# Kernel tuning notes

Measured on AMD Instinct MI355X. Metric: run time of the kernel, lower is better.

The kernel has to match this reference:

```python
import jax, jax.numpy as jnp
import numpy as np

ALPHA = 0.2  # LeakyReLU negative slope


def _gat_layer(h, dst, adj, w, a_in, a_out, b):
    # h: [N, F_in], dst: [N, K] int (edge (i,k): i -> dst[i,k]), adj: [N, K]
    hid = h @ w                      # [N, D]
    s_in = hid @ a_in                # [N]  (attention applied to source-node half)
    s_out = hid @ a_out              # [N]  (attention applied to dest-node half)
    # edge scores, grouped per source node (matches view(-1, num_neighs) softmax)
    e = jax.nn.leaky_relu(s_in[:, None] + s_out[dst], ALPHA)   # [N, K]
    # torch code detaches attention (Variable(..., requires_grad=False))
    att = jax.lax.stop_gradient(jax.nn.softmax(e, axis=1))     # [N, K]
    w_edge = adj * att                                          # [N, K]
    # SpMM: out[i] = sum_k w_edge[i,k] * hid[dst[i,k]]
    out = jnp.einsum('nk,nkd->nd', w_edge, hid[dst]) + b        # [N, D]
    return out


def setup_inputs() -> dict:
    key = jax.random.key(0)
    ks = jax.random.split(key, 12)
    N, K, F, H, O = 100000, 16, 128, 128, 128
    stdv1 = 1.0 / np.sqrt(H)
    stdv2 = 1.0 / np.sqrt(O)
    u = lambda k, shp, s: jax.random.uniform(k, shp, jnp.float32, -s, s)
    return {
        'x': jax.random.normal(ks[0], (N, F), jnp.float32),
        'dst_idx': jax.random.randint(ks[1], (N, K), 0, N),
        'adj_vals': jax.random.uniform(ks[2], (N, K), jnp.float32),
        'w1': u(ks[3], (F, H), stdv1),
        'a_in1': jax.random.normal(ks[4], (H,), jnp.float32) * (1.414 / np.sqrt(H)),
        'a_out1': jax.random.normal(ks[5], (H,), jnp.float32) * (1.414 / np.sqrt(H)),
        'b1': u(ks[6], (H,), stdv1),
        'w2': u(ks[7], (H, O), stdv2),
        'a_in2': jax.random.normal(ks[8], (O,), jnp.float32) * (1.414 / np.sqrt(O)),
        'a_out2': jax.random.normal(ks[9], (O,), jnp.float32) * (1.414 / np.sqrt(O)),
        'b2': u(ks[10], (O,), stdv2),
    }


def reference(x, dst_idx, adj_vals, w1, a_in1, a_out1, b1, w2, a_in2, a_out2, b2):
    h = jax.nn.relu(_gat_layer(x, dst_idx, adj_vals, w1, a_in1, a_out1, b1))
    h = jax.nn.relu(_gat_layer(h, dst_idx, adj_vals, w2, a_in2, a_out2, b2))
    return h
```

## Files before the change

### kernel.cpp

```cpp
#include <hip/hip_runtime.h>

#define ALPHA 0.2f
#define LDA 136

typedef short bf16x8 __attribute__((ext_vector_type(8)));
typedef float f32x4  __attribute__((ext_vector_type(4)));

static __device__ __forceinline__ float bf2f(unsigned short u) {
    union { unsigned int i; float f; } v; v.i = ((unsigned int)u) << 16; return v.f;
}
static __device__ __forceinline__ unsigned short f2bf(float f) {
    union { float f; unsigned int i; } v; v.f = f;
    unsigned int x = v.i;
    return (unsigned short)((x + 0x7fffu + ((x >> 16) & 1u)) >> 16);
}

__global__ __launch_bounds__(256)
void prep_wT_kernel(const float* __restrict__ w1, const float* __restrict__ w2,
                    unsigned short* __restrict__ wT1, unsigned short* __restrict__ wT2)
{
    __shared__ unsigned short wL[128 * 130];
    const float* w = blockIdx.x ? w2 : w1;
    unsigned short* wT = blockIdx.x ? wT2 : wT1;
    const int tid = threadIdx.x;

    for (int i = 0; i < 16; i++) {
        int e = tid + i * 256;
        int k = e >> 5, c0 = (e & 31) * 4;
        float4 v = *(const float4*)&w[k * 128 + c0];
        wL[(c0 + 0) * 130 + k] = f2bf(v.x);
        wL[(c0 + 1) * 130 + k] = f2bf(v.y);
        wL[(c0 + 2) * 130 + k] = f2bf(v.z);
        wL[(c0 + 3) * 130 + k] = f2bf(v.w);
    }
    __syncthreads();
    for (int i = 0; i < 8; i++) {
        int e = tid + i * 256;
        int c = e >> 4, k0 = (e & 15) * 8;
        ushort4 a, b;
        a.x = wL[c * 130 + k0 + 0]; a.y = wL[c * 130 + k0 + 1];
        a.z = wL[c * 130 + k0 + 2]; a.w = wL[c * 130 + k0 + 3];
        b.x = wL[c * 130 + k0 + 4]; b.y = wL[c * 130 + k0 + 5];
        b.z = wL[c * 130 + k0 + 6]; b.w = wL[c * 130 + k0 + 7];
        *(ushort4*)&wT[c * 128 + k0]     = a;
        *(ushort4*)&wT[c * 128 + k0 + 4] = b;
    }
}

template <bool SRC_BF>
__global__ __launch_bounds__(256)
void gemm_score_mfma(const void* __restrict__ srcv,
                     const unsigned short* __restrict__ wT,
                     const float* __restrict__ a_in,
                     const float* __restrict__ a_out,
                     unsigned short* __restrict__ hid,
                     float* __restrict__ s_in,
                     float* __restrict__ s_out,
                     int n)
{
    __shared__ short As[64 * LDA];
    __shared__ short Bs[128 * LDA];
    __shared__ float aS[2][128];

    const int tid = threadIdx.x;
    const int rbase = blockIdx.x * 64;

    if (tid < 128) { aS[0][tid] = a_in[tid]; aS[1][tid] = a_out[tid]; }

    if (SRC_BF) {
        const unsigned short* src = (const unsigned short*)srcv;
        #pragma unroll
        for (int i = 0; i < 8; i++) {
            int e = tid + i * 256;
            int r = e >> 5, c4 = (e & 31) * 4;
            int gr = rbase + r;
            ushort4 v;
            if (gr < n) v = *(const ushort4*)&src[(size_t)gr * 128 + c4];
            else { v.x = v.y = v.z = v.w = 0; }
            *(ushort4*)&As[r * LDA + c4] = v;
        }
    } else {
        const float* src = (const float*)srcv;
        #pragma unroll
        for (int i = 0; i < 8; i++) {
            int e = tid + i * 256;
            int r = e >> 5, c4 = (e & 31) * 4;
            int gr = rbase + r;
            ushort4 u;
            if (gr < n) {
                float4 v = *(const float4*)&src[(size_t)gr * 128 + c4];
                u.x = f2bf(v.x); u.y = f2bf(v.y); u.z = f2bf(v.z); u.w = f2bf(v.w);
            } else { u.x = u.y = u.z = u.w = 0; }
            *(ushort4*)&As[r * LDA + c4] = u;
        }
    }
    #pragma unroll
    for (int i = 0; i < 8; i++) {
        int e = tid + i * 256;
        int nr = e >> 4, j = (e & 15) * 8;
        int4 v = *(const int4*)&wT[nr * 128 + j];
        *(int4*)&Bs[nr * LDA + j] = v;
    }
    __syncthreads();

    const int lane = tid & 63;
    const int wv = tid >> 6;
    const int m = lane & 15;
    const int q = lane >> 4;

    f32x4 acc[8];
    #pragma unroll
    for (int t = 0; t < 8; t++) acc[t] = (f32x4){0.f, 0.f, 0.f, 0.f};

    const short* Abase = &As[(wv * 16 + m) * LDA + q * 8];
    const short* Bbase = &Bs[m * LDA + q * 8];

    #pragma unroll
    for (int ks = 0; ks < 4; ks++) {
        bf16x8 aF = *(const bf16x8*)(Abase + ks * 32);
        #pragma unroll
        for (int t = 0; t < 8; t++) {
            bf16x8 bF = *(const bf16x8*)(Bbase + t * 16 * LDA + ks * 32);
            acc[t] = __builtin_amdgcn_mfma_f32_16x16x32_bf16(aF, bF, acc[t], 0, 0, 0);
        }
    }

    float pin[4] = {0.f, 0.f, 0.f, 0.f}, pout[4] = {0.f, 0.f, 0.f, 0.f};
    #pragma unroll
    for (int t = 0; t < 8; t++) {
        float ai = aS[0][t * 16 + m];
        float ao = aS[1][t * 16 + m];
        #pragma unroll
        for (int r = 0; r < 4; r++) {
            pin[r]  += acc[t][r] * ai;
            pout[r] += acc[t][r] * ao;
        }
    }
    #pragma unroll
    for (int msk = 8; msk >= 1; msk >>= 1) {
        #pragma unroll
        for (int r = 0; r < 4; r++) {
            pin[r]  += __shfl_xor(pin[r],  msk);
            pout[r] += __shfl_xor(pout[r], msk);
        }
    }
    if (m == 0) {
        #pragma unroll
        for (int r = 0; r < 4; r++) {
            int g = rbase + wv * 16 + q * 4 + r;
            if (g < n) { s_in[g] = pin[r]; s_out[g] = pout[r]; }
        }
    }

    #pragma unroll
    for (int t = 0; t < 8; t++)
        #pragma unroll
        for (int r = 0; r < 4; r++)
            As[(wv * 16 + q * 4 + r) * LDA + t * 16 + m] = (short)f2bf(acc[t][r]);
    __syncthreads();
    #pragma unroll
    for (int i = 0; i < 4; i++) {
        int e = tid + i * 256;
        int r = e >> 4, j = (e & 15) * 8;
        int gr = rbase + r;
        if (gr < n) {
            int4 v = *(const int4*)&As[r * LDA + j];
            *(int4*)&hid[(size_t)gr * 128 + j] = v;
        }
    }
}

template <bool FINAL>
__global__ __launch_bounds__(256)
void gat_aggregate_kernel(const unsigned short* __restrict__ hid,
                          const float* __restrict__ s_in,
                          const float* __restrict__ s_out,
                          const int* __restrict__ dst,
                          const float* __restrict__ adj,
                          const float* __restrict__ bias,
                          void* __restrict__ outv,
                          int n)
{
    const int lane = threadIdx.x & 63;
    const int node = (blockIdx.x * 256 + threadIdx.x) >> 6;
    if (node >= n) return;

    float sc = -1e30f;
    int dk = 0;
    float av = 0.f;
    if (lane < 16) {
        int ei = node * 16 + lane;
        dk = dst[ei];
        av = adj[ei];
        float e = s_in[node] + s_out[dk];
        sc = (e > 0.f) ? e : ALPHA * e;
    }
    float m = sc;
    #pragma unroll
    for (int msk = 8; msk >= 1; msk >>= 1) m = fmaxf(m, __shfl_xor(m, msk));
    float p = (lane < 16) ? __expf(sc - m) : 0.f;
    float s = p;
    #pragma unroll
    for (int msk = 8; msk >= 1; msk >>= 1) s += __shfl_xor(s, msk);
    float wk = (lane < 16) ? av * p / s : 0.f;

    const int c = lane * 2;
    float accx = 0.f, accy = 0.f;
    #pragma unroll
    for (int k = 0; k < 16; k++) {
        float wkk = __shfl(wk, k);
        int   dkk = __shfl(dk, k);
        ushort2 hq = *(const ushort2*)&hid[(size_t)dkk * 128 + c];
        accx += wkk * bf2f(hq.x);
        accy += wkk * bf2f(hq.y);
    }
    float ox = fmaxf(accx + bias[c],     0.f);
    float oy = fmaxf(accy + bias[c + 1], 0.f);

    const size_t oidx = (size_t)node * 128 + c;
    if (FINAL) {
        *(float2*)&((float*)outv)[oidx] = make_float2(ox, oy);
    } else {
        ushort2 ov; ov.x = f2bf(ox); ov.y = f2bf(oy);
        *(ushort2*)&((unsigned short*)outv)[oidx] = ov;
    }
}

extern "C" void kernel_launch(void* const* d_in, const int* in_sizes, int n_in,
                              void* d_out, int out_size, void* d_ws, size_t ws_size,
                              hipStream_t stream)
{
    const float* x      = (const float*)d_in[0];
    const int*   dst    = (const int*)d_in[1];
    const float* adj    = (const float*)d_in[2];
    const float* w1     = (const float*)d_in[3];
    const float* a_in1  = (const float*)d_in[4];
    const float* a_out1 = (const float*)d_in[5];
    const float* b1     = (const float*)d_in[6];
    const float* w2     = (const float*)d_in[7];
    const float* a_in2  = (const float*)d_in[8];
    const float* a_out2 = (const float*)d_in[9];
    const float* b2     = (const float*)d_in[10];

    const int N = in_sizes[0] / 128;

    unsigned short* hid   = (unsigned short*)d_ws;
    float*          s_in  = (float*)(hid + (size_t)N * 128);
    float*          s_out = s_in + N;
    unsigned short* wT1   = (unsigned short*)(s_out + N);
    unsigned short* wT2   = wT1 + 128 * 128;
    unsigned short* h1    = (unsigned short*)d_out + out_size;

    dim3 blk(256);
    dim3 ggrid((N + 63) / 64);
    dim3 agrid((N + 3) / 4);

    prep_wT_kernel<<<2, blk, 0, stream>>>(w1, w2, wT1, wT2);

    gemm_score_mfma<false><<<ggrid, blk, 0, stream>>>(x,  wT1, a_in1, a_out1,
                                                      hid, s_in, s_out, N);
    gat_aggregate_kernel<false><<<agrid, blk, 0, stream>>>(hid, s_in, s_out, dst,
                                                           adj, b1, h1, N);
    gemm_score_mfma<true><<<ggrid, blk, 0, stream>>>(h1, wT2, a_in2, a_out2,
                                                     hid, s_in, s_out, N);
    gat_aggregate_kernel<true><<<agrid, blk, 0, stream>>>(hid, s_in, s_out, dst,
                                                          adj, b2, d_out, N);
}
```

Before: 267.3 us.

## Split edge softmax into separate fully-parallel kernel before gather

Moves the per-edge attention softmax out of the aggregation kernel into its own kernel, which uses all 64 lanes of a wavefront (four nodes per wave) and writes normalized edge weights to a workspace buffer. The gather kernel then loads indices and weights with vector loads and drops the shuffles. This avoids the aggregation kernel spending a serialized softmax phase where 48 of 64 lanes sit idle. In exchange it adds two kernel launches and an extra write and read of an N x 16 float buffer per layer.

Measured after the change: 284.9 us. +6.6%, slower.

```diff
diff --git a/kernel.cpp b/kernel.cpp
--- a/kernel.cpp
+++ b/kernel.cpp
@@ -170,49 +170,65 @@
     }
 }
 
+__global__ __launch_bounds__(256)
+void edge_weights_kernel(const float* __restrict__ s_in,
+                         const float* __restrict__ s_out,
+                         const int* __restrict__ dst,
+                         const float* __restrict__ adj,
+                         float* __restrict__ we,
+                         int n)
+{
+    const int idx = blockIdx.x * 256 + threadIdx.x;
+    const int node = idx >> 4;
+    if (node >= n) return;
+
+    const int dk = dst[idx];
+    float t = s_in[node] + s_out[dk];
+    float e = (t > 0.f) ? t : ALPHA * t;
+
+    float m = e;
+    #pragma unroll
+    for (int msk = 8; msk >= 1; msk >>= 1) m = fmaxf(m, __shfl_xor(m, msk));
+    float p = __expf(e - m);
+    float s = p;
+    #pragma unroll
+    for (int msk = 8; msk >= 1; msk >>= 1) s += __shfl_xor(s, msk);
+
+    we[idx] = adj[idx] * p / s;
+}
+
 template <bool FINAL>
 __global__ __launch_bounds__(256)
-void gat_aggregate_kernel(const unsigned short* __restrict__ hid,
-                          const float* __restrict__ s_in,
-                          const float* __restrict__ s_out,
-                          const int* __restrict__ dst,
-                          const float* __restrict__ adj,
-                          const float* __restrict__ bias,
-                          void* __restrict__ outv,
-                          int n)
+void gat_gather_kernel(const unsigned short* __restrict__ hid,
+                       const int* __restrict__ dst,
+                       const float* __restrict__ we,
+                       const float* __restrict__ bias,
+                       void* __restrict__ outv,
+                       int n)
 {
     const int lane = threadIdx.x & 63;
     const int node = (blockIdx.x * 256 + threadIdx.x) >> 6;
     if (node >= n) return;
 
-    float sc = -1e30f;
-    int dk = 0;
-    float av = 0.f;
-    if (lane < 16) {
-        int ei = node * 16 + lane;
-        dk = dst[ei];
-        av = adj[ei];
-        float e = s_in[node] + s_out[dk];
-        sc = (e > 0.f) ? e : ALPHA * e;
-    }
-    float m = sc;
-    #pragma unroll
-    for (int msk = 8; msk >= 1; msk >>= 1) m = fmaxf(m, __shfl_xor(m, msk));
-    float p = (lane < 16) ? __expf(sc - m) : 0.f;
-    float s = p;
-    #pragma unroll
-    for (int msk = 8; msk >= 1; msk >>= 1) s += __shfl_xor(s, msk);
-    float wk = (lane < 16) ? av * p / s : 0.f;
+    int dk[16];
+    float wk[16];
+    #pragma unroll
+    for (int j = 0; j < 4; j++) {
+        int4   dv = *(const int4*)&dst[node * 16 + j * 4];
+        float4 wv = *(const float4*)&we[node * 16 + j * 4];
+        dk[j * 4 + 0] = dv.x; dk[j * 4 + 1] = dv.y;
+        dk[j * 4 + 2] = dv.z; dk[j * 4 + 3] = dv.w;
+        wk[j * 4 + 0] = wv.x; wk[j * 4 + 1] = wv.y;
+        wk[j * 4 + 2] = wv.z; wk[j * 4 + 3] = wv.w;
+    }
 
     const int c = lane * 2;
     float accx = 0.f, accy = 0.f;
     #pragma unroll
     for (int k = 0; k < 16; k++) {
-        float wkk = __shfl(wk, k);
-        int   dkk = __shfl(dk, k);
-        ushort2 hq = *(const ushort2*)&hid[(size_t)dkk * 128 + c];
-        accx += wkk * bf2f(hq.x);
-        accy += wkk * bf2f(hq.y);
+        ushort2 hq = *(const ushort2*)&hid[(size_t)dk[k] * 128 + c];
+        accx += wk[k] * bf2f(hq.x);
+        accy += wk[k] * bf2f(hq.y);
     }
     float ox = fmaxf(accx + bias[c],     0.f);
     float oy = fmaxf(accy + bias[c + 1], 0.f);
@@ -247,22 +263,24 @@
     unsigned short* hid   = (unsigned short*)d_ws;
     float*          s_in  = (float*)(hid + (size_t)N * 128);
     float*          s_out = s_in + N;
-    unsigned short* wT1   = (unsigned short*)(s_out + N);
+    float*          we    = s_out + N;
+    unsigned short* wT1   = (unsigned short*)(we + (size_t)N * 16);
     unsigned short* wT2   = wT1 + 128 * 128;
     unsigned short* h1    = (unsigned short*)d_out + out_size;
 
     dim3 blk(256);
     dim3 ggrid((N + 63) / 64);
+    dim3 egrid((N * 16 + 255) / 256);
     dim3 agrid((N + 3) / 4);
 
     prep_wT_kernel<<<2, blk, 0, stream>>>(w1, w2, wT1, wT2);
 
     gemm_score_mfma<false><<<ggrid, blk, 0, stream>>>(x,  wT1, a_in1, a_out1,
                                                       hid, s_in, s_out, N);
-    gat_aggregate_kernel<false><<<agrid, blk, 0, stream>>>(hid, s_in, s_out, dst,
-                                                           adj, b1, h1, N);
+    edge_weights_kernel<<<egrid, blk, 0, stream>>>(s_in, s_out, dst, adj, we, N);
+    gat_gather_kernel<false><<<agrid, blk, 0, stream>>>(hid, dst, we, b1, h1, N);
     gemm_score_mfma<true><<<ggrid, blk, 0, stream>>>(h1, wT2, a_in2, a_out2,
                                                      hid, s_in, s_out, N);
-    gat_aggregate_kernel<true><<<agrid, blk, 0, stream>>>(hid, s_in, s_out, dst,
-                                                          adj, b2, d_out, N);
-}
+    edge_weights_kernel<<<egrid, blk, 0, stream>>>(s_in, s_out, dst, adj, we, N);
+    gat_gather_kernel<true><<<agrid, blk, 0, stream>>>(hid, dst, we, b2, d_out, N);
+}
```
